# Performance work log

Measured on AMD Instinct MI355X. Metric: run time of the kernel, lower is better.

## Reference

```python
import jax, jax.numpy as jnp
import numpy as np

LN_EPS = 1e-5

def _layernorm(x, g, b):
    m = jnp.mean(x, axis=-1, keepdims=True)
    v = jnp.mean((x - m) ** 2, axis=-1, keepdims=True)
    return (x - m) / jnp.sqrt(v + LN_EPS) * g + b

def _mlp(x, w1, g1, b1, w2, g2, b2):
    # Linear(no bias) -> LayerNorm -> Linear(no bias) -> LayerNorm -> ReLU
    x = _layernorm(x @ w1, g1, b1)
    x = _layernorm(x @ w2, g2, b2)
    return jax.nn.relu(x)

def setup_inputs() -> dict:
    key = jax.random.key(0)
    ks = jax.random.split(key, 16)
    Lc, Lf, N, Dc, Df, K = 1024, 4096, 32, 256, 128, 8
    inv = lambda d: 1.0 / np.sqrt(d)
    inp = {
        "features_coarse": jax.random.normal(ks[0], (Lc, N, Dc), dtype=jnp.float32),
        "features_fine": jax.random.normal(ks[1], (Lf, N, Df), dtype=jnp.float32),
        # mlp_coarse: d_in=Dc, d_ff=Df, d_out=Df
        "w1c": jax.random.uniform(ks[2], (Dc, Df), jnp.float32, -inv(Dc), inv(Dc)),
        "g1c": jnp.ones((Df,), jnp.float32),
        "b1c": jnp.zeros((Df,), jnp.float32),
        "w2c": jax.random.uniform(ks[3], (Df, Df), jnp.float32, -inv(Df), inv(Df)),
        "g2c": jnp.ones((Df,), jnp.float32),
        "b2c": jnp.zeros((Df,), jnp.float32),
        # mlp_fine: d_in=Df, d_ff=Df, d_out=Df
        "w1f": jax.random.uniform(ks[4], (Df, Df), jnp.float32, -inv(Df), inv(Df)),
        "g1f": jnp.ones((Df,), jnp.float32),
        "b1f": jnp.zeros((Df,), jnp.float32),
        "w2f": jax.random.uniform(ks[5], (Df, Df), jnp.float32, -inv(Df), inv(Df)),
        "g2f": jnp.ones((Df,), jnp.float32),
        "b2f": jnp.zeros((Df,), jnp.float32),
        "neighbor_row": jax.random.randint(ks[6], (K * Lc * N,), 0, Lf, dtype=jnp.int64 if jax.config.jax_enable_x64 else jnp.int32),
        "neighbor_col": jax.random.randint(ks[7], (K * Lc * N,), 0, N, dtype=jnp.int64 if jax.config.jax_enable_x64 else jnp.int32),
        "keep_idx": jax.random.randint(ks[8], (Lc,), 0, Lf, dtype=jnp.int64 if jax.config.jax_enable_x64 else jnp.int32),
    }
    return inp

def reference(features_coarse, features_fine, w1c, g1c, b1c, w2c, g2c, b2c,
              w1f, g1f, b1f, w2f, g2f, b2f, neighbor_row, neighbor_col, keep_idx):
    Lc, N, Dc = features_coarse.shape
    Lf, _, Df = features_fine.shape
    D = Df
    fc = _mlp(features_coarse, w1c, g1c, b1c, w2c, g2c, b2c)  # (Lc, N, D)
    ff = _mlp(features_fine, w1f, g1f, b1f, w2f, g2f, b2f)    # (Lf, N, D)
    gathered = ff[neighbor_row, neighbor_col]                  # (K*Lc*N, D)
    updated = fc[None] + gathered.reshape(-1, Lc, N, D)        # (K, Lc, N, D)
    ff = ff.at[neighbor_row, neighbor_col].set(updated.reshape(-1, D))
    return ff
```

## Files before the change

kernel.cpp:

```cpp
#include <hip/hip_runtime.h>
#include <hip/hip_bf16.h>

typedef __attribute__((ext_vector_type(8))) short s8v;
typedef __attribute__((ext_vector_type(4))) float f4v;

__device__ __forceinline__ short f2bf(float f) {
    __hip_bfloat16 h = __float2bfloat16(f);
    union { __hip_bfloat16 h; short s; } u{h};
    return u.s;
}
__device__ __forceinline__ float bf2f(unsigned short v) {
    union { unsigned u; float f; } x; x.u = ((unsigned)v) << 16; return x.f;
}
__device__ __forceinline__ unsigned packbf(float a, float b) {
    return (unsigned)(unsigned short)f2bf(a) | ((unsigned)(unsigned short)f2bf(b) << 16);
}

__global__ void prep_kernel(const float* __restrict__ w1c, const float* __restrict__ w2c,
                            const float* __restrict__ g1c, const float* __restrict__ b1c,
                            const float* __restrict__ w1f, const float* __restrict__ w2f,
                            const float* __restrict__ g1f, const float* __restrict__ b1f,
                            short* __restrict__ p1c, short* __restrict__ p2c,
                            short* __restrict__ p1f, short* __restrict__ p2f,
                            float* __restrict__ s2c, float* __restrict__ bwc,
                            float* __restrict__ s2f, float* __restrict__ bwf,
                            int* __restrict__ win)
{
    int b = blockIdx.x, t = threadIdx.x;
    if (b >= 42) {
        int idx4 = (b - 42) * 256 + t;
        int4 z; z.x = 0; z.y = 0; z.z = 0; z.w = 0;
        *(int4*)(win + idx4 * 4) = z;
        return;
    }
    if (b >= 40) {
        if (t >= 128) return;
        const float* W  = (b == 40) ? w2c : w2f;
        const float* g1 = (b == 40) ? g1c : g1f;
        const float* b1 = (b == 40) ? b1c : b1f;
        float* s2 = (b == 40) ? s2c : s2f;
        float* bw = (b == 40) ? bwc : bwf;
        float s = 0.f, w2sum = 0.f;
        for (int k = 0; k < 128; ++k) {
            float wv = W[k * 128 + t];
            s     += bf2f((unsigned short)f2bf(g1[k] * wv));
            w2sum += b1[k] * wv;
        }
        s2[t] = s; bw[t] = w2sum;
        return;
    }
    int id = b * 256 + t;
    int f  = id >> 6, l = id & 63;
    const float* W; const float* g1 = nullptr; short* P; int fl;
    if      (f < 64)  { W = w1c; P = p1c; fl = f; }
    else if (f < 96)  { W = w2c; P = p2c; fl = f - 64;  g1 = g1c; }
    else if (f < 128) { W = w1f; P = p1f; fl = f - 96; }
    else              { W = w2f; P = p2f; fl = f - 128; g1 = g1f; }
    int g = l >> 4, c = l & 15;
    int ks = fl >> 3, n = fl & 7;
    s8v o;
    #pragma unroll
    for (int e = 0; e < 8; ++e) {
        int k = ks*32 + g*8 + e;
        float v = W[k * 128 + n*16 + c];
        if (g1) v *= g1[k];
        o[e] = f2bf(v);
    }
    *(s8v*)(P + ((fl*64 + l) << 3)) = o;
}

__global__ __launch_bounds__(512, 4)
void coarse_mlp(const float* __restrict__ X,
                const short* __restrict__ WpA, const short* __restrict__ WpB,
                const float* __restrict__ s2v, const float* __restrict__ bwv,
                const float* __restrict__ g2v, const float* __restrict__ b2v,
                unsigned short* __restrict__ outB,
                const int* __restrict__ nr, const int* __restrict__ nc,
                int* __restrict__ win, int nWinBlocks)
{
    __shared__ short Ws[32768];

    if (blockIdx.x < (unsigned)nWinBlocks) {
        int i = blockIdx.x * 512 + threadIdx.x;
        atomicMax(&win[nr[i] * 32 + nc[i]], i + 1);
        return;
    }
    const int bid  = blockIdx.x - nWinBlocks;
    const int tid  = threadIdx.x;
    const int lane = tid & 63;
    const int wave = tid >> 6;
    const int G = lane >> 4, n16 = lane & 15;
    const int row = bid * 128 + wave * 16 + n16;
    const size_t rowK = (size_t)row * 256;

    #pragma unroll
    for (int r = 0; r < 8; ++r) {
        int ch = r*512 + tid;
        *(s8v*)&Ws[ch*8] = *(const s8v*)(WpA + (size_t)ch*8);
    }

    const float* pX = X + rowK + G*8;
    float4 aPf[4][2];
    #pragma unroll
    for (int k2 = 0; k2 < 4; ++k2) {
        aPf[k2][0] = *(const float4*)(pX + k2*32);
        aPf[k2][1] = *(const float4*)(pX + k2*32 + 4);
    }
    __syncthreads();

    f4v acc1[8];
    #pragma unroll
    for (int mt = 0; mt < 8; ++mt) acc1[mt] = (f4v){0.f, 0.f, 0.f, 0.f};

    #pragma unroll
    for (int kb = 0; kb < 8; kb += 4) {
        #pragma unroll
        for (int k2 = 0; k2 < 4; ++k2) {
            const int ks = kb + k2;
            s8v wfr[8];
            #pragma unroll
            for (int mt = 0; mt < 8; ++mt)
                wfr[mt] = *(const s8v*)&Ws[((ks*8 + mt)*64 + lane) * 8];
            s8v xf;
            xf[0] = f2bf(aPf[k2][0].x); xf[1] = f2bf(aPf[k2][0].y);
            xf[2] = f2bf(aPf[k2][0].z); xf[3] = f2bf(aPf[k2][0].w);
            xf[4] = f2bf(aPf[k2][1].x); xf[5] = f2bf(aPf[k2][1].y);
            xf[6] = f2bf(aPf[k2][1].z); xf[7] = f2bf(aPf[k2][1].w);
            #pragma unroll
            for (int mt = 0; mt < 8; ++mt)
                acc1[mt] = __builtin_amdgcn_mfma_f32_16x16x32_bf16(wfr[mt], xf, acc1[mt], 0, 0, 0);
        }
        if (kb + 4 < 8) {
            #pragma unroll
            for (int k2 = 0; k2 < 4; ++k2) {
                aPf[k2][0] = *(const float4*)(pX + (kb+4+k2)*32);
                aPf[k2][1] = *(const float4*)(pX + (kb+4+k2)*32 + 4);
            }
        }
    }

    __syncthreads();
    #pragma unroll
    for (int r = 0; r < 4; ++r) {
        int ch = r*512 + tid;
        *(s8v*)&Ws[ch*8] = *(const s8v*)(WpB + (size_t)ch*8);
    }
    __syncthreads();

    float sm = 0.f, sq = 0.f;
    #pragma unroll
    for (int mt = 0; mt < 8; ++mt)
        #pragma unroll
        for (int j = 0; j < 4; ++j) { float v = acc1[mt][j]; sm += v; sq += v*v; }
    sm += __shfl_xor(sm, 16, 64); sm += __shfl_xor(sm, 32, 64);
    sq += __shfl_xor(sq, 16, 64); sq += __shfl_xor(sq, 32, 64);
    const float mean1 = sm * (1.f/128.f);
    const float rstd1 = rsqrtf(sq * (1.f/128.f) - mean1*mean1 + 1e-5f);

    unsigned pk[8][2];
    #pragma unroll
    for (int mt = 0; mt < 8; ++mt) {
        pk[mt][0] = packbf(acc1[mt][0], acc1[mt][1]);
        pk[mt][1] = packbf(acc1[mt][2], acc1[mt][3]);
    }

    f4v acc2[8];
    #pragma unroll
    for (int mt = 0; mt < 8; ++mt) acc2[mt] = (f4v){0.f, 0.f, 0.f, 0.f};

    const int src0 = ((G & 1) << 5) + n16;
    const int src1 = src0 + 16;
    const bool hiG = (G >= 2);
    #pragma unroll
    for (int ks = 0; ks < 4; ++ks) {
        int r00 = __shfl((int)pk[2*ks][0],   src0, 64);
        int r01 = __shfl((int)pk[2*ks][1],   src0, 64);
        int r02 = __shfl((int)pk[2*ks][0],   src1, 64);
        int r03 = __shfl((int)pk[2*ks][1],   src1, 64);
        int r10 = __shfl((int)pk[2*ks+1][0], src0, 64);
        int r11 = __shfl((int)pk[2*ks+1][1], src0, 64);
        int r12 = __shfl((int)pk[2*ks+1][0], src1, 64);
        int r13 = __shfl((int)pk[2*ks+1][1], src1, 64);
        union { int u[4]; s8v v; } hb;
        hb.u[0] = hiG ? r10 : r00; hb.u[1] = hiG ? r11 : r01;
        hb.u[2] = hiG ? r12 : r02; hb.u[3] = hiG ? r13 : r03;
        s8v wfr[8];
        #pragma unroll
        for (int mt = 0; mt < 8; ++mt)
            wfr[mt] = *(const s8v*)&Ws[((ks*8 + mt)*64 + lane) * 8];
        #pragma unroll
        for (int mt = 0; mt < 8; ++mt)
            acc2[mt] = __builtin_amdgcn_mfma_f32_16x16x32_bf16(wfr[mt], hb.v, acc2[mt], 0, 0, 0);
    }

    float h2[8][4];
    float sm2 = 0.f, sq2 = 0.f;
    #pragma unroll
    for (int mt = 0; mt < 8; ++mt) {
        const int col = mt*16 + G*4;
        f4v s2l = *(const f4v*)&s2v[col];
        f4v bwl = *(const f4v*)&bwv[col];
        #pragma unroll
        for (int j = 0; j < 4; ++j) {
            float v = rstd1 * (acc2[mt][j] - mean1 * s2l[j]) + bwl[j];
            h2[mt][j] = v; sm2 += v; sq2 += v*v;
        }
    }
    sm2 += __shfl_xor(sm2, 16, 64); sm2 += __shfl_xor(sm2, 32, 64);
    sq2 += __shfl_xor(sq2, 16, 64); sq2 += __shfl_xor(sq2, 32, 64);
    const float mean2 = sm2 * (1.f/128.f);
    const float rstd2 = rsqrtf(sq2 * (1.f/128.f) - mean2*mean2 + 1e-5f);

    #pragma unroll
    for (int mt = 0; mt < 8; ++mt) {
        const int col = mt*16 + G*4;
        f4v g2l = *(const f4v*)&g2v[col];
        f4v b2l = *(const f4v*)&b2v[col];
        ushort4 o;
        o.x = (unsigned short)f2bf(fmaxf((h2[mt][0]-mean2)*rstd2*g2l[0] + b2l[0], 0.f));
        o.y = (unsigned short)f2bf(fmaxf((h2[mt][1]-mean2)*rstd2*g2l[1] + b2l[1], 0.f));
        o.z = (unsigned short)f2bf(fmaxf((h2[mt][2]-mean2)*rstd2*g2l[2] + b2l[2], 0.f));
        o.w = (unsigned short)f2bf(fmaxf((h2[mt][3]-mean2)*rstd2*g2l[3] + b2l[3], 0.f));
        *(ushort4*)(outB + (size_t)row * 128 + col) = o;
    }
}

__global__ __launch_bounds__(512, 4)
void fine_mlp(const float* __restrict__ X,
              const short* __restrict__ WpA, const short* __restrict__ WpB,
              const float* __restrict__ s2v, const float* __restrict__ bwv,
              const float* __restrict__ g2v, const float* __restrict__ b2v,
              float* __restrict__ out,
              const int* __restrict__ winner,
              const unsigned short* __restrict__ fcB)
{
    __shared__ short Ws[32768];
    __shared__ short Xs[8192];

    const int tid  = threadIdx.x;
    const int wave = tid >> 6, lane = tid & 63;
    const int G = lane >> 4, n16 = lane & 15;
    const int row0 = blockIdx.x * 128;
    const int rloc = wave * 16 + n16;
    const int row  = row0 + rloc;
    char* xs = (char*)Xs;

    #pragma unroll
    for (int r = 0; r < 4; ++r) {
        int ch = r*512 + tid;
        *(s8v*)&Ws[ch*8] = *(const s8v*)(WpA + (size_t)ch*8);
    }
    #pragma unroll
    for (int r = 0; r < 4; ++r) {
        int ch = r*512 + tid;
        *(s8v*)&Ws[16384 + ch*8] = *(const s8v*)(WpB + (size_t)ch*8);
    }

    #pragma unroll
    for (int it = 0; it < 4; ++it) {
        int i  = it*512 + tid;
        int r  = i >> 4;
        int c4 = i & 15;
        float4 v = *(const float4*)(X + (size_t)(row0 + r) * 128 + c4*4);
        uint2 p; p.x = packbf(v.x, v.y); p.y = packbf(v.z, v.w);
        int pg = (c4 >> 1) ^ (r & 7);
        *(uint2*)(xs + r*128 + pg*16 + (c4 & 1)*8) = p;
    }
    int wv = winner[row];
    __syncthreads();

    f4v acc[8];
    #pragma unroll
    for (int mt = 0; mt < 8; ++mt) acc[mt] = (f4v){0.f, 0.f, 0.f, 0.f};

    #pragma unroll
    for (int ks = 0; ks < 2; ++ks) {
        int pg = (ks*4 + G) ^ (rloc & 7);
        s8v xf = *(const s8v*)(xs + rloc*128 + pg*16);
        s8v wfr[8];
        #pragma unroll
        for (int mt = 0; mt < 8; ++mt)
            wfr[mt] = *(const s8v*)&Ws[((ks*8 + mt)*64 + lane) * 8];
        #pragma unroll
        for (int mt = 0; mt < 8; ++mt)
            acc[mt] = __builtin_amdgcn_mfma_f32_16x16x32_bf16(wfr[mt], xf, acc[mt], 0, 0, 0);
    }
    __syncthreads();

    #pragma unroll
    for (int it = 0; it < 4; ++it) {
        int i  = it*512 + tid;
        int r  = i >> 4;
        int c4 = i & 15;
        float4 v = *(const float4*)(X + (size_t)(row0 + r) * 128 + 64 + c4*4);
        uint2 p; p.x = packbf(v.x, v.y); p.y = packbf(v.z, v.w);
        int pg = (c4 >> 1) ^ (r & 7);
        *(uint2*)(xs + r*128 + pg*16 + (c4 & 1)*8) = p;
    }
    s8v gv[2][2];
    int wrr[2];
    {
        const int g8 = lane & 7;
        #pragma unroll
        for (int it = 0; it < 2; ++it) {
            int rr = it*8 + (lane >> 3);
            int w  = __shfl(wv, rr, 64);
            wrr[it] = w;
            size_t src = (size_t)((w > 0 ? w - 1 : 0) & 32767) * 128;
            #pragma unroll
            for (int ch = 0; ch < 2; ++ch)
                gv[it][ch] = *(const s8v*)(fcB + src + ch*64 + g8*8);
        }
    }
    __syncthreads();

    #pragma unroll
    for (int ks = 2; ks < 4; ++ks) {
        int pg = ((ks-2)*4 + G) ^ (rloc & 7);
        s8v xf = *(const s8v*)(xs + rloc*128 + pg*16);
        s8v wfr[8];
        #pragma unroll
        for (int mt = 0; mt < 8; ++mt)
            wfr[mt] = *(const s8v*)&Ws[((ks*8 + mt)*64 + lane) * 8];
        #pragma unroll
        for (int mt = 0; mt < 8; ++mt)
            acc[mt] = __builtin_amdgcn_mfma_f32_16x16x32_bf16(wfr[mt], xf, acc[mt], 0, 0, 0);
    }

    float sm = 0.f, sq = 0.f;
    #pragma unroll
    for (int mt = 0; mt < 8; ++mt)
        #pragma unroll
        for (int j = 0; j < 4; ++j) { float v = acc[mt][j]; sm += v; sq += v*v; }
    sm += __shfl_xor(sm, 16, 64); sm += __shfl_xor(sm, 32, 64);
    sq += __shfl_xor(sq, 16, 64); sq += __shfl_xor(sq, 32, 64);
    const float mean1 = sm * (1.f/128.f);
    const float rstd1 = rsqrtf(sq * (1.f/128.f) - mean1*mean1 + 1e-5f);

    unsigned pk[8][2];
    #pragma unroll
    for (int mt = 0; mt < 8; ++mt) {
        pk[mt][0] = packbf(acc[mt][0], acc[mt][1]);
        pk[mt][1] = packbf(acc[mt][2], acc[mt][3]);
        acc[mt] = (f4v){0.f, 0.f, 0.f, 0.f};
    }

    const int src0 = ((G & 1) << 5) + n16;
    const int src1 = src0 + 16;
    const bool hiG = (G >= 2);
    #pragma unroll
    for (int ks = 0; ks < 4; ++ks) {
        int r00 = __shfl((int)pk[2*ks][0],   src0, 64);
        int r01 = __shfl((int)pk[2*ks][1],   src0, 64);
        int r02 = __shfl((int)pk[2*ks][0],   src1, 64);
        int r03 = __shfl((int)pk[2*ks][1],   src1, 64);
        int r10 = __shfl((int)pk[2*ks+1][0], src0, 64);
        int r11 = __shfl((int)pk[2*ks+1][1], src0, 64);
        int r12 = __shfl((int)pk[2*ks+1][0], src1, 64);
        int r13 = __shfl((int)pk[2*ks+1][1], src1, 64);
        union { int u[4]; s8v v; } hb;
        hb.u[0] = hiG ? r10 : r00; hb.u[1] = hiG ? r11 : r01;
        hb.u[2] = hiG ? r12 : r02; hb.u[3] = hiG ? r13 : r03;
        s8v wfr[8];
        #pragma unroll
        for (int mt = 0; mt < 8; ++mt)
            wfr[mt] = *(const s8v*)&Ws[16384 + ((ks*8 + mt)*64 + lane) * 8];
        #pragma unroll
        for (int mt = 0; mt < 8; ++mt)
            acc[mt] = __builtin_amdgcn_mfma_f32_16x16x32_bf16(wfr[mt], hb.v, acc[mt], 0, 0, 0);
    }

    float h2[8][4];
    float sm2 = 0.f, sq2 = 0.f;
    #pragma unroll
    for (int mt = 0; mt < 8; ++mt) {
        const int col = mt*16 + G*4;
        f4v s2l = *(const f4v*)&s2v[col];
        f4v bwl = *(const f4v*)&bwv[col];
        #pragma unroll
        for (int j = 0; j < 4; ++j) {
            float v = rstd1 * (acc[mt][j] - mean1 * s2l[j]) + bwl[j];
            h2[mt][j] = v; sm2 += v; sq2 += v*v;
        }
    }
    sm2 += __shfl_xor(sm2, 16, 64); sm2 += __shfl_xor(sm2, 32, 64);
    sq2 += __shfl_xor(sq2, 16, 64); sq2 += __shfl_xor(sq2, 32, 64);
    const float mean2 = sm2 * (1.f/128.f);
    const float rstd2 = rsqrtf(sq2 * (1.f/128.f) - mean2*mean2 + 1e-5f);

    #pragma unroll
    for (int ch = 0; ch < 2; ++ch) {
        #pragma unroll
        for (int mtL = 0; mtL < 4; ++mtL) {
            const int mt = ch*4 + mtL;
            const int col = mt*16 + G*4;
            f4v g2l = *(const f4v*)&g2v[col];
            f4v b2l = *(const f4v*)&b2v[col];
            float z0 = fmaxf((h2[mt][0]-mean2)*rstd2*g2l[0] + b2l[0], 0.f);
            float z1 = fmaxf((h2[mt][1]-mean2)*rstd2*g2l[1] + b2l[1], 0.f);
            float z2 = fmaxf((h2[mt][2]-mean2)*rstd2*g2l[2] + b2l[2], 0.f);
            float z3 = fmaxf((h2[mt][3]-mean2)*rstd2*g2l[3] + b2l[3], 0.f);
            uint2 p; p.x = packbf(z0, z1); p.y = packbf(z2, z3);
            int pg = (mtL*2 + (G >> 1)) ^ (rloc & 7);
            *(uint2*)(xs + rloc*128 + pg*16 + (G & 1)*8) = p;
        }
        asm volatile("s_waitcnt lgkmcnt(0)" ::: "memory");
        #pragma unroll
        for (int it = 0; it < 2; ++it) {
            const int g8  = lane & 7;
            const int rr  = it*8 + (lane >> 3);
            const int rl2 = wave*16 + rr;
            int pg = g8 ^ (rr & 7);
            s8v v = *(const s8v*)(xs + rl2*128 + pg*16);
            float y[8];
            #pragma unroll
            for (int e = 0; e < 8; ++e) y[e] = bf2f((unsigned short)v[e]);
            if (wrr[it] > 0) {
                #pragma unroll
                for (int e = 0; e < 8; ++e) y[e] += bf2f((unsigned short)gv[it][ch][e]);
            }
            float4 o0 = {y[0], y[1], y[2], y[3]};
            float4 o1 = {y[4], y[5], y[6], y[7]};
            float* op = out + (size_t)(row0 + rl2) * 128 + ch*64 + g8*8;
            *(float4*)op       = o0;
            *(float4*)(op + 4) = o1;
        }
        asm volatile("" ::: "memory");
    }
}

extern "C" void kernel_launch(void* const* d_in, const int* in_sizes, int n_in,
                              void* d_out, int out_size, void* d_ws, size_t ws_size,
                              hipStream_t stream)
{
    const float* fcoarse = (const float*)d_in[0];
    const float* ffine   = (const float*)d_in[1];
    const float* w1c = (const float*)d_in[2];
    const float* g1c = (const float*)d_in[3];
    const float* b1c = (const float*)d_in[4];
    const float* w2c = (const float*)d_in[5];
    const float* g2c = (const float*)d_in[6];
    const float* b2c = (const float*)d_in[7];
    const float* w1f = (const float*)d_in[8];
    const float* g1f = (const float*)d_in[9];
    const float* b1f = (const float*)d_in[10];
    const float* w2f = (const float*)d_in[11];
    const float* g2f = (const float*)d_in[12];
    const float* b2f = (const float*)d_in[13];
    const int* nrow  = (const int*)d_in[14];
    const int* ncol  = (const int*)d_in[15];

    float* out = (float*)d_out;
    const int Mc = 32768, Mf = 131072;

    unsigned short* fcB = (unsigned short*)d_ws;
    char* base = (char*)d_ws;
    int*   winner = (int*)(base + 8u*1024*1024);
    short* p1c = (short*)(base + 8u*1024*1024 + 512u*1024);
    short* p2c = p1c + 256*128;
    short* p1f = p2c + 128*128;
    short* p2f = p1f + 128*128;
    float* s2c = (float*)(p2f + 128*128);
    float* bwc = s2c + 128;
    float* s2f = bwc + 128;
    float* bwf = s2f + 128;

    prep_kernel<<<170, 256, 0, stream>>>(w1c, w2c, g1c, b1c, w1f, w2f, g1f, b1f,
                                         p1c, p2c, p1f, p2f, s2c, bwc, s2f, bwf,
                                         winner);

    coarse_mlp<<<512 + Mc/128, 512, 0, stream>>>(
        fcoarse, p1c, p2c, s2c, bwc, g2c, b2c, fcB,
        nrow, ncol, winner, 512);

    fine_mlp<<<Mf/128, 512, 0, stream>>>(
        ffine, p1f, p2f, s2f, bwf, g2f, b2f,
        out, winner, fcB);
}
```

Before: 70.26 us.

## Pre-convert fine features to bf16 in coarse kernel; load fragments directly

```diff
diff --git a/kernel.cpp b/kernel.cpp
--- a/kernel.cpp
+++ b/kernel.cpp
@@ -70,22 +70,35 @@
 }
 
 __global__ __launch_bounds__(512, 4)
-void coarse_mlp(const float* __restrict__ X,
-                const short* __restrict__ WpA, const short* __restrict__ WpB,
-                const float* __restrict__ s2v, const float* __restrict__ bwv,
-                const float* __restrict__ g2v, const float* __restrict__ b2v,
-                unsigned short* __restrict__ outB,
-                const int* __restrict__ nr, const int* __restrict__ nc,
-                int* __restrict__ win, int nWinBlocks)
+void coarse_mega(const float* __restrict__ X,
+                 const short* __restrict__ WpA, const short* __restrict__ WpB,
+                 const float* __restrict__ s2v, const float* __restrict__ bwv,
+                 const float* __restrict__ g2v, const float* __restrict__ b2v,
+                 unsigned short* __restrict__ outB,
+                 const int* __restrict__ nr, const int* __restrict__ nc,
+                 int* __restrict__ win,
+                 const float* __restrict__ Xf, unsigned short* __restrict__ Xbf)
 {
     __shared__ short Ws[32768];
 
-    if (blockIdx.x < (unsigned)nWinBlocks) {
+    if (blockIdx.x < 512) {
         int i = blockIdx.x * 512 + threadIdx.x;
         atomicMax(&win[nr[i] * 32 + nc[i]], i + 1);
         return;
     }
-    const int bid  = blockIdx.x - nWinBlocks;
+    if (blockIdx.x >= 768) {
+        int b = blockIdx.x - 768;
+        int t = threadIdx.x;
+        #pragma unroll
+        for (int it = 0; it < 8; ++it) {
+            int idx4 = b*4096 + it*512 + t;
+            float4 v = *(const float4*)(Xf + (size_t)idx4 * 4);
+            uint2 p; p.x = packbf(v.x, v.y); p.y = packbf(v.z, v.w);
+            *(uint2*)(Xbf + (size_t)idx4 * 4) = p;
+        }
+        return;
+    }
+    const int bid  = blockIdx.x - 512;
     const int tid  = threadIdx.x;
     const int lane = tid & 63;
     const int wave = tid >> 6;
@@ -226,7 +239,7 @@
 }
 
 __global__ __launch_bounds__(512, 4)
-void fine_mlp(const float* __restrict__ X,
+void fine_mlp(const unsigned short* __restrict__ Xbf,
               const short* __restrict__ WpA, const short* __restrict__ WpB,
               const float* __restrict__ s2v, const float* __restrict__ bwv,
               const float* __restrict__ g2v, const float* __restrict__ b2v,
@@ -246,57 +259,20 @@
     char* xs = (char*)Xs;
 
     #pragma unroll
-    for (int r = 0; r < 4; ++r) {
+    for (int r = 0; r < 8; ++r) {
         int ch = r*512 + tid;
         *(s8v*)&Ws[ch*8] = *(const s8v*)(WpA + (size_t)ch*8);
     }
-    #pragma unroll
-    for (int r = 0; r < 4; ++r) {
-        int ch = r*512 + tid;
-        *(s8v*)&Ws[16384 + ch*8] = *(const s8v*)(WpB + (size_t)ch*8);
-    }
-
-    #pragma unroll
-    for (int it = 0; it < 4; ++it) {
-        int i  = it*512 + tid;
-        int r  = i >> 4;
-        int c4 = i & 15;
-        float4 v = *(const float4*)(X + (size_t)(row0 + r) * 128 + c4*4);
-        uint2 p; p.x = packbf(v.x, v.y); p.y = packbf(v.z, v.w);
-        int pg = (c4 >> 1) ^ (r & 7);
-        *(uint2*)(xs + r*128 + pg*16 + (c4 & 1)*8) = p;
+    s8v xf[4];
+    {
+        const unsigned short* pX = Xbf + (size_t)row * 128 + G*8;
+        #pragma unroll
+        for (int ks = 0; ks < 4; ++ks)
+            xf[ks] = *(const s8v*)(pX + ks*32);
     }
     int wv = winner[row];
     __syncthreads();
 
-    f4v acc[8];
-    #pragma unroll
-    for (int mt = 0; mt < 8; ++mt) acc[mt] = (f4v){0.f, 0.f, 0.f, 0.f};
-
-    #pragma unroll
-    for (int ks = 0; ks < 2; ++ks) {
-        int pg = (ks*4 + G) ^ (rloc & 7);
-        s8v xf = *(const s8v*)(xs + rloc*128 + pg*16);
-        s8v wfr[8];
-        #pragma unroll
-        for (int mt = 0; mt < 8; ++mt)
-            wfr[mt] = *(const s8v*)&Ws[((ks*8 + mt)*64 + lane) * 8];
-        #pragma unroll
-        for (int mt = 0; mt < 8; ++mt)
-            acc[mt] = __builtin_amdgcn_mfma_f32_16x16x32_bf16(wfr[mt], xf, acc[mt], 0, 0, 0);
-    }
-    __syncthreads();
-
-    #pragma unroll
-    for (int it = 0; it < 4; ++it) {
-        int i  = it*512 + tid;
-        int r  = i >> 4;
-        int c4 = i & 15;
-        float4 v = *(const float4*)(X + (size_t)(row0 + r) * 128 + 64 + c4*4);
-        uint2 p; p.x = packbf(v.x, v.y); p.y = packbf(v.z, v.w);
-        int pg = (c4 >> 1) ^ (r & 7);
-        *(uint2*)(xs + r*128 + pg*16 + (c4 & 1)*8) = p;
-    }
     s8v gv[2][2];
     int wrr[2];
     {
@@ -312,19 +288,20 @@
                 gv[it][ch] = *(const s8v*)(fcB + src + ch*64 + g8*8);
         }
     }
-    __syncthreads();
-
-    #pragma unroll
-    for (int ks = 2; ks < 4; ++ks) {
-        int pg = ((ks-2)*4 + G) ^ (rloc & 7);
-        s8v xf = *(const s8v*)(xs + rloc*128 + pg*16);
+
+    f4v acc[8];
+    #pragma unroll
+    for (int mt = 0; mt < 8; ++mt) acc[mt] = (f4v){0.f, 0.f, 0.f, 0.f};
+
+    #pragma unroll
+    for (int ks = 0; ks < 4; ++ks) {
         s8v wfr[8];
         #pragma unroll
         for (int mt = 0; mt < 8; ++mt)
             wfr[mt] = *(const s8v*)&Ws[((ks*8 + mt)*64 + lane) * 8];
         #pragma unroll
         for (int mt = 0; mt < 8; ++mt)
-            acc[mt] = __builtin_amdgcn_mfma_f32_16x16x32_bf16(wfr[mt], xf, acc[mt], 0, 0, 0);
+            acc[mt] = __builtin_amdgcn_mfma_f32_16x16x32_bf16(wfr[mt], xf[ks], acc[mt], 0, 0, 0);
     }
 
     float sm = 0.f, sq = 0.f;
@@ -464,16 +441,17 @@
     float* bwc = s2c + 128;
     float* s2f = bwc + 128;
     float* bwf = s2f + 128;
+    unsigned short* Xbf = (unsigned short*)(base + 9078784u);
 
     prep_kernel<<<170, 256, 0, stream>>>(w1c, w2c, g1c, b1c, w1f, w2f, g1f, b1f,
                                          p1c, p2c, p1f, p2f, s2c, bwc, s2f, bwf,
                                          winner);
 
-    coarse_mlp<<<512 + Mc/128, 512, 0, stream>>>(
+    coarse_mega<<<1792, 512, 0, stream>>>(
         fcoarse, p1c, p2c, s2c, bwc, g2c, b2c, fcB,
-        nrow, ncol, winner, 512);
+        nrow, ncol, winner, ffine, Xbf);
 
     fine_mlp<<<Mf/128, 512, 0, stream>>>(
-        ffine, p1f, p2f, s2f, bwf, g2f, b2f,
+        Xbf, p1f, p2f, s2f, bwf, g2f, b2f,
         out, winner, fcB);
 }
```

After: 74.35 us. +5.8%, slower.
